# Kernel optimization log

Hardware: AMD Instinct MI355X
Metric: run time of the kernel (lower is better)

## Reference

```python
import jax, jax.numpy as jnp
import numpy as np

DIM = 1024
HEADS = 16
HEAD_DIM = DIM // HEADS


def setup_inputs() -> dict:
    key = jax.random.key(0)
    ks = jax.random.split(key, 5)
    B, N = 4, 2048
    x = jax.random.normal(ks[0], (B, N, DIM), dtype=jnp.float32)
    # nn.Linear default init scale ~ 1/sqrt(fan_in)
    s = 1.0 / np.sqrt(DIM)
    W_qkv = jax.random.uniform(ks[1], (DIM, 3 * DIM), minval=-s, maxval=s, dtype=jnp.float32)
    b_qkv = jax.random.uniform(ks[2], (3 * DIM,), minval=-s, maxval=s, dtype=jnp.float32)
    W_proj = jax.random.uniform(ks[3], (DIM, DIM), minval=-s, maxval=s, dtype=jnp.float32)
    b_proj = jax.random.uniform(ks[4], (DIM,), minval=-s, maxval=s, dtype=jnp.float32)
    return {"x": x, "W_qkv": W_qkv, "b_qkv": b_qkv, "W_proj": W_proj, "b_proj": b_proj}


def reference(x, W_qkv, b_qkv, W_proj, b_proj):
    B, N, C = x.shape
    qkv = x @ W_qkv + b_qkv                      # [B, N, 3C]
    qkv = qkv.reshape(B, N, 3, HEADS, HEAD_DIM)
    q = jnp.transpose(qkv[:, :, 0], (0, 2, 1, 3))  # [B, H, N, D]
    k = jnp.transpose(qkv[:, :, 1], (0, 2, 1, 3))
    v = jnp.transpose(qkv[:, :, 2], (0, 2, 1, 3))
    scale = 1.0 / np.sqrt(HEAD_DIM)
    scores = jnp.einsum('bhqd,bhkd->bhqk', q, k) * scale  # [B, H, N, N]
    attn = jax.nn.softmax(scores, axis=-1)
    out = jnp.einsum('bhqk,bhkd->bhqd', attn, v)           # [B, H, N, D]
    out = jnp.transpose(out, (0, 2, 1, 3)).reshape(B, N, C)
    return out @ W_proj + b_proj
```

## Files before the change

kernel.cpp:

```cpp
#include <hip/hip_runtime.h>

typedef __attribute__((ext_vector_type(2)))  float  f32x2;
typedef __attribute__((ext_vector_type(4)))  float  f32x4;
typedef __attribute__((ext_vector_type(16))) float  f32x16;
typedef __attribute__((ext_vector_type(8)))  short  short8;
typedef __attribute__((ext_vector_type(4)))  unsigned int u32x4;
typedef __attribute__((ext_vector_type(2)))  unsigned int uint2v;

#define MFMA16 __builtin_amdgcn_mfma_f32_16x16x32_bf16
#define MFMA32 __builtin_amdgcn_mfma_f32_32x32x16_bf16

static __device__ __forceinline__ unsigned short f2bf(float f){
  union { float f; unsigned u; } v; v.f = f;
  unsigned r = v.u + 0x7fffu + ((v.u >> 16) & 1u);
  return (unsigned short)(r >> 16);
}

static __device__ __forceinline__ unsigned cvtpk(float a, float b){
  unsigned r;
  asm("v_cvt_pk_bf16_f32 %0, %1, %2" : "=v"(r) : "v"(a), "v"(b));
  return r;
}

static __device__ __forceinline__ void plswap(unsigned &a, unsigned &b){
  asm("v_permlane32_swap_b32 %0, %1" : "+v"(a), "+v"(b));
}

typedef __attribute__((address_space(1))) void gvoid_t;
typedef __attribute__((address_space(3))) void lvoid_t;

static __device__ __forceinline__ void gll16(const unsigned short* g, unsigned short* l){
  __builtin_amdgcn_global_load_lds((gvoid_t*)g, (lvoid_t*)l, 16, 0, 0);
}


__global__ __launch_bounds__(256) void k_convert(const float* __restrict__ x,
                                                 unsigned short* __restrict__ xb){
  __shared__ __align__(16) unsigned short sm[16384];
  const int mblk = blockIdx.x >> 4, kt = blockIdx.x & 15;
  const int t = threadIdx.x;
  const int l16 = t & 15, rg = t >> 4;
  #pragma unroll
  for (int p = 0; p < 16; p++){
    int row = p * 16 + rg;
    f32x4 v = *(const f32x4*)&x[(size_t)(mblk*256 + row) * 1024 + kt*64 + l16*4];
    uint2v u; u[0] = cvtpk(v[0], v[1]); u[1] = cvtpk(v[2], v[3]);
    int g = l16 >> 1;
    *(uint2v*)&sm[row*64 + ((g ^ (row & 7)) << 3) + (l16 & 1)*4] = u;
  }
  __syncthreads();
  size_t obase = (size_t)((mblk*16 + kt)*2) * 8192;
  #pragma unroll
  for (int i = 0; i < 8; i++){
    int o = i * 256 + t;
    int kh = o >> 10, rem = o & 1023;
    int band = rem >> 6, cc = (rem >> 4) & 3, ri = rem & 15;
    int r = band*16 + ri, g = kh*4 + cc;
    short8 vv = *(const short8*)&sm[r*64 + ((g ^ (r & 7)) << 3)];
    *(short8*)&xb[obase + (size_t)kh*8192 + rem*8] = vv;
  }
}

__global__ __launch_bounds__(256) void k_transpose(const float* __restrict__ W,
                                                   unsigned short* __restrict__ Wt,
                                                   int K, int N){
  __shared__ float tile[32][33];
  int n0 = blockIdx.x * 32, k0 = blockIdx.y * 32;
  int tx = threadIdx.x, ty = threadIdx.y;
  #pragma unroll
  for (int r = 0; r < 4; r++)
    tile[ty + 8*r][tx] = W[(size_t)(k0 + ty + 8*r) * N + n0 + tx];
  __syncthreads();
  #pragma unroll
  for (int r = 0; r < 4; r++){
    int nn = ty + 8*r;
    int n = n0 + nn, k = k0 + tx;
    int kt = k >> 6, kh = (k >> 5) & 1, cc = (k >> 3) & 3, ke = k & 7;
    int nblk = n >> 8, band = (n & 255) >> 4, ri = n & 15;
    Wt[(size_t)(((nblk*16 + kt)*2 + kh)) * 8192 + band*512 + cc*128 + ri*8 + ke] =
        f2bf(tile[tx][nn]);
  }
}

#define VMW(N) { __builtin_amdgcn_sched_barrier(0);                        \
                 asm volatile("s_waitcnt vmcnt(" #N ")" ::: "memory");     \
                 __builtin_amdgcn_s_barrier();                             \
                 __builtin_amdgcn_sched_barrier(0); }

template<int MODE>
__global__ __launch_bounds__(512, 2) void k_gemm(const unsigned short* __restrict__ A,
                                                 const unsigned short* __restrict__ Bt,
                                                 const float* __restrict__ bias,
                                                 void* __restrict__ outp,
                                                 int NT){
  __shared__ __align__(16) unsigned short lds[49152];
  const int t = threadIdx.x, w = t >> 6, l = t & 63;
  const int wr = w >> 2, wc = w & 3;
  const int bx = blockIdx.x, by = blockIdx.y;
  const int mblk = bx >> 1, mhalf = bx & 1;

  const unsigned short* Ab = A + (size_t)mblk*262144 + mhalf*4096 + t*8;
  const unsigned short* Bb = Bt + (size_t)by*262144 + t*8;

  f32x4 acc[4][4];
  #pragma unroll
  for (int i = 0; i < 4; i++)
    #pragma unroll
    for (int j = 0; j < 4; j++)
      acc[i][j] = (f32x4){0.f, 0.f, 0.f, 0.f};

  auto stage = [&](int sl){
    const int b = sl & 3;
    const size_t off = (size_t)sl * 8192;
    gll16(Ab + off,        &lds[b*12288 + t*8]);
    gll16(Bb + off,        &lds[b*12288 + 4096 + t*8]);
    gll16(Bb + off + 4096, &lds[b*12288 + 8192 + t*8]);
  };

  auto phase = [&](int b, bool do_stage, int sl){
    short8 af[4], bfr[4];
    const int aoff = b*12288 + wr*2048 + l*8;
    const int boff = b*12288 + 4096 + wc*2048 + l*8;
    #pragma unroll
    for (int i = 0; i < 4; i++) af[i]  = *(const short8*)&lds[aoff + i*512];
    #pragma unroll
    for (int j = 0; j < 4; j++) bfr[j] = *(const short8*)&lds[boff + j*512];
    if (do_stage) stage(sl);
    __builtin_amdgcn_sched_barrier(0);
    __builtin_amdgcn_s_barrier();
    __builtin_amdgcn_s_setprio(1);
    #pragma unroll
    for (int i = 0; i < 4; i++)
      #pragma unroll
      for (int j = 0; j < 4; j++)
        acc[i][j] = MFMA16(af[i], bfr[j], acc[i][j], 0, 0, 0);
    __builtin_amdgcn_s_setprio(0);
  };

  stage(0); stage(1); stage(2);
  VMW(6);

  const int NP = 2 * NT;
  int p = 0;
  for (; p <= NP - 4; ++p){
    phase(p & 3, true, p + 3);
    VMW(6);
  }
  phase(p & 3, false, 0); VMW(3); ++p;
  phase(p & 3, false, 0); VMW(0); ++p;
  phase(p & 3, false, 0);

  if (MODE == 0){
    unsigned short* qg = (unsigned short*)outp;
    unsigned short* kg = qg + (size_t)8388608;
    unsigned short* vg = kg + (size_t)8388608;
    const int which = by >> 2;
    const int lrow = l & 15;
    #pragma unroll
    for (int j = 0; j < 4; j++){
      int col = by*256 + wc*64 + j*16 + lrow;
      float bi = bias[col];
      int cc = col & 1023;
      int h = cc >> 6;
      int d = j*16 + lrow;
      if (which == 2){
        int db = d >> 5, dd = d & 31;
        #pragma unroll
        for (int i = 0; i < 4; i++){
          int nn = bx*128 + wr*64 + i*16 + (l >> 4)*4;
          int b = nn >> 11, key = nn & 2047;
          size_t idx = (size_t)(key >> 6)*4096 + (size_t)(((key >> 4) & 3)*2 + db)*512
                     + (((key >> 3) & 1)*32 + dd)*8 + (key & 7);
          uint2v u;
          u[0] = cvtpk(acc[i][j][0] + bi, acc[i][j][1] + bi);
          u[1] = cvtpk(acc[i][j][2] + bi, acc[i][j][3] + bi);
          *(uint2v*)&vg[(size_t)(b*16 + h)*131072 + idx] = u;
        }
      } else {
        unsigned short* dst = which ? kg : qg;
        float scale = which ? 1.0f : 0.18033688011f;
        int dsub = (d >> 4)*512 + ((d >> 3) & 1)*256 + (d & 7);
        #pragma unroll
        for (int i = 0; i < 4; i++)
          #pragma unroll
          for (int reg = 0; reg < 4; reg++){
            int nn = bx*128 + wr*64 + i*16 + (l >> 4)*4 + reg;
            int b = nn >> 11, row = nn & 2047;
            dst[(size_t)(b*16 + h)*131072 + (size_t)(row >> 5)*2048 + dsub + (row & 31)*8] =
                f2bf((acc[i][j][reg] + bi) * scale);
          }
      }
    }
  } else {
    float* out = (float*)outp;
    #pragma unroll
    for (int i = 0; i < 4; i++)
      #pragma unroll
      for (int reg = 0; reg < 4; reg++){
        int row = bx*128 + wr*64 + i*16 + (l >> 4)*4 + reg;
        #pragma unroll
        for (int j = 0; j < 4; j++){
          int col = by*256 + wc*64 + j*16 + (l & 15);
          out[(size_t)row * 1024 + col] = acc[i][j][reg] + bias[col];
        }
      }
  }
}

__global__ __launch_bounds__(256, 2) void k_attn(const unsigned short* __restrict__ Qg,
                                                 const unsigned short* __restrict__ Kg,
                                                 const unsigned short* __restrict__ Vg,
                                                 unsigned short* __restrict__ aout){
  __shared__ __align__(16) unsigned short lds[20480];

  const int t = threadIdx.x, w = t >> 6, l = t & 63;
  const int hi = l >> 5, q31 = l & 31;
  const int d0 = blockIdx.x;
  const int xcd = d0 & 7, jj = d0 >> 3;
  const int bh = xcd + 8*(jj >> 3);
  const int bx = jj & 7;

  const unsigned short* Qp = Qg + (size_t)bh*131072 + (size_t)bx*16384;
  const unsigned short* Kp = Kg + (size_t)bh*131072;
  const unsigned short* Vp = Vg + (size_t)bh*131072;

  #pragma unroll
  for (int i = 0; i < 8; i++){ int c = i*256 + t; gll16(Qp + c*8, &lds[c*8]); }
  {
    short8 z8 = {0,0,0,0,0,0,0,0};
    *(short8*)&lds[16384 + t*16]     = z8;
    *(short8*)&lds[16384 + t*16 + 8] = z8;
  }
  __syncthreads();
  short8 qf0[4], qf1[4];
  #pragma unroll
  for (int ds = 0; ds < 4; ds++){
    qf0[ds] = *(const short8*)&lds[(2*w + 0)*2048 + ds*512 + l*8];
    qf1[ds] = *(const short8*)&lds[(2*w + 1)*2048 + ds*512 + l*8];
  }
  __syncthreads();

  #pragma unroll
  for (int i = 0; i < 2; i++){
    int c = i*256 + t;
    gll16(Kp + c*8, &lds[c*8]);
    gll16(Vp + c*8, &lds[8192 + c*8]);
  }
  __syncthreads();

  f32x16 ZERO;
  #pragma unroll
  for (int i = 0; i < 16; i++) ZERO[i] = 0.f;
  f32x16 o0lo = ZERO, o0hi = ZERO, o1lo = ZERO, o1hi = ZERO;
  float lsum0 = 0.f, lsum1 = 0.f;
  u32x4 pA0[4], pA1[4], pB0[4], pB1[4];
  #pragma unroll
  for (int ks = 0; ks < 4; ks++){
    pA0[ks][0]=0u; pA0[ks][1]=0u; pA0[ks][2]=0u; pA0[ks][3]=0u;
    pA1[ks][0]=0u; pA1[ks][1]=0u; pA1[ks][2]=0u; pA1[ks][3]=0u;
  }
  int s0 = 0, s1 = 1, s2 = 2;

  auto body = [&](int kt, u32x4 (&pO0)[4], u32x4 (&pO1)[4],
                          u32x4 (&pN0)[4], u32x4 (&pN1)[4]){
    const int cbk = (kt & 1) * 4096;
    if (kt < 31){
      const int nbk = cbk ^ 4096;
      const int nv  = 8192 + s1*4096;
      #pragma unroll
      for (int i = 0; i < 2; i++){
        int c = i*256 + t;
        gll16(Kp + (size_t)(kt + 1)*4096 + c*8, &lds[nbk + c*8]);
        gll16(Vp + (size_t)(kt + 1)*4096 + c*8, &lds[nv + c*8]);
      }
    }

    f32x16 sA0, sB0, sA1, sB1;
    __builtin_amdgcn_s_setprio(1);
    {
      short8 kfA = *(const short8*)&lds[cbk + l*8];
      short8 kfB = *(const short8*)&lds[cbk + 2048 + l*8];
      sA0 = MFMA32(kfA, qf0[0], ZERO, 0, 0, 0);
      sB0 = MFMA32(kfB, qf0[0], ZERO, 0, 0, 0);
      sA1 = MFMA32(kfA, qf1[0], ZERO, 0, 0, 0);
      sB1 = MFMA32(kfB, qf1[0], ZERO, 0, 0, 0);
    }
    #pragma unroll
    for (int ds = 1; ds < 4; ds++){
      short8 kfA = *(const short8*)&lds[cbk + ds*512 + l*8];
      short8 kfB = *(const short8*)&lds[cbk + 2048 + ds*512 + l*8];
      sA0 = MFMA32(kfA, qf0[ds], sA0, 0, 0, 0);
      sB0 = MFMA32(kfB, qf0[ds], sB0, 0, 0, 0);
      sA1 = MFMA32(kfA, qf1[ds], sA1, 0, 0, 0);
      sB1 = MFMA32(kfB, qf1[ds], sB1, 0, 0, 0);
    }
    __builtin_amdgcn_s_setprio(0);
    __builtin_amdgcn_sched_barrier(0);

    const int pvb = 8192 + s2*4096;

    #pragma unroll
    for (int i = 0; i < 16; i++){
      sA0[i] = __builtin_amdgcn_exp2f(sA0[i]);
      sB0[i] = __builtin_amdgcn_exp2f(sB0[i]);
      sA1[i] = __builtin_amdgcn_exp2f(sA1[i]);
      sB1[i] = __builtin_amdgcn_exp2f(sB1[i]);
    }
    lsum0 += ((((sA0[0]+sA0[1])+(sA0[2]+sA0[3])) + ((sA0[4]+sA0[5])+(sA0[6]+sA0[7])))
           +  (((sA0[8]+sA0[9])+(sA0[10]+sA0[11])) + ((sA0[12]+sA0[13])+(sA0[14]+sA0[15]))))
           + ((((sB0[0]+sB0[1])+(sB0[2]+sB0[3])) + ((sB0[4]+sB0[5])+(sB0[6]+sB0[7])))
           +  (((sB0[8]+sB0[9])+(sB0[10]+sB0[11])) + ((sB0[12]+sB0[13])+(sB0[14]+sB0[15]))));
    lsum1 += ((((sA1[0]+sA1[1])+(sA1[2]+sA1[3])) + ((sA1[4]+sA1[5])+(sA1[6]+sA1[7])))
           +  (((sA1[8]+sA1[9])+(sA1[10]+sA1[11])) + ((sA1[12]+sA1[13])+(sA1[14]+sA1[15]))))
           + ((((sB1[0]+sB1[1])+(sB1[2]+sB1[3])) + ((sB1[4]+sB1[5])+(sB1[6]+sB1[7])))
           +  (((sB1[8]+sB1[9])+(sB1[10]+sB1[11])) + ((sB1[12]+sB1[13])+(sB1[14]+sB1[15]))));

    {
      unsigned wA[8], wB[8];
      #pragma unroll
      for (int j = 0; j < 8; j++){ wA[j] = cvtpk(sA0[2*j], sA0[2*j+1]); wB[j] = cvtpk(sB0[2*j], sB0[2*j+1]); }
      { unsigned a=wA[0],b=wA[2]; plswap(a,b); pN0[0][0]=a; pN0[0][2]=b; }
      { unsigned a=wA[1],b=wA[3]; plswap(a,b); pN0[0][1]=a; pN0[0][3]=b; }
      { unsigned a=wA[4],b=wA[6]; plswap(a,b); pN0[1][0]=a; pN0[1][2]=b; }
      { unsigned a=wA[5],b=wA[7]; plswap(a,b); pN0[1][1]=a; pN0[1][3]=b; }
      { unsigned a=wB[0],b=wB[2]; plswap(a,b); pN0[2][0]=a; pN0[2][2]=b; }
      { unsigned a=wB[1],b=wB[3]; plswap(a,b); pN0[2][1]=a; pN0[2][3]=b; }
      { unsigned a=wB[4],b=wB[6]; plswap(a,b); pN0[3][0]=a; pN0[3][2]=b; }
      { unsigned a=wB[5],b=wB[7]; plswap(a,b); pN0[3][1]=a; pN0[3][3]=b; }
    }
    {
      unsigned wA[8], wB[8];
      #pragma unroll
      for (int j = 0; j < 8; j++){ wA[j] = cvtpk(sA1[2*j], sA1[2*j+1]); wB[j] = cvtpk(sB1[2*j], sB1[2*j+1]); }
      { unsigned a=wA[0],b=wA[2]; plswap(a,b); pN1[0][0]=a; pN1[0][2]=b; }
      { unsigned a=wA[1],b=wA[3]; plswap(a,b); pN1[0][1]=a; pN1[0][3]=b; }
      { unsigned a=wA[4],b=wA[6]; plswap(a,b); pN1[1][0]=a; pN1[1][2]=b; }
      { unsigned a=wA[5],b=wA[7]; plswap(a,b); pN1[1][1]=a; pN1[1][3]=b; }
      { unsigned a=wB[0],b=wB[2]; plswap(a,b); pN1[2][0]=a; pN1[2][2]=b; }
      { unsigned a=wB[1],b=wB[3]; plswap(a,b); pN1[2][1]=a; pN1[2][3]=b; }
      { unsigned a=wB[4],b=wB[6]; plswap(a,b); pN1[3][0]=a; pN1[3][2]=b; }
      { unsigned a=wB[5],b=wB[7]; plswap(a,b); pN1[3][1]=a; pN1[3][3]=b; }
    }

    #pragma unroll
    for (int ks = 0; ks < 4; ks++){
      short8 p0r, p1r;
      *(u32x4*)&p0r = pO0[ks];
      *(u32x4*)&p1r = pO1[ks];
      short8 vf0 = *(const short8*)&lds[pvb + (ks*2 + 0)*512 + l*8];
      short8 vf1 = *(const short8*)&lds[pvb + (ks*2 + 1)*512 + l*8];
      o0lo = MFMA32(vf0, p0r, o0lo, 0, 0, 0);
      o0hi = MFMA32(vf1, p0r, o0hi, 0, 0, 0);
      o1lo = MFMA32(vf0, p1r, o1lo, 0, 0, 0);
      o1hi = MFMA32(vf1, p1r, o1hi, 0, 0, 0);
    }

    #pragma unroll
    for (int g4 = 0; g4 < 4; g4++){
      __builtin_amdgcn_sched_group_barrier(0x100, 2, 0);
      __builtin_amdgcn_sched_group_barrier(0x002, 40, 0);
      __builtin_amdgcn_sched_group_barrier(0x008, 4, 0);
    }
    __builtin_amdgcn_sched_group_barrier(0x002, 64, 0);

    __syncthreads();
    int tmp = s2; s2 = s0; s0 = s1; s1 = tmp;
  };

  for (int kt2 = 0; kt2 < 32; kt2 += 2){
    body(kt2,     pA0, pA1, pB0, pB1);
    body(kt2 + 1, pB0, pB1, pA0, pA1);
  }

  {
    const int pvb = 8192 + s2*4096;
    __builtin_amdgcn_s_setprio(1);
    #pragma unroll
    for (int ks = 0; ks < 4; ks++){
      short8 p0r, p1r;
      *(u32x4*)&p0r = pA0[ks];
      *(u32x4*)&p1r = pA1[ks];
      short8 vf0 = *(const short8*)&lds[pvb + (ks*2 + 0)*512 + l*8];
      short8 vf1 = *(const short8*)&lds[pvb + (ks*2 + 1)*512 + l*8];
      o0lo = MFMA32(vf0, p0r, o0lo, 0, 0, 0);
      o0hi = MFMA32(vf1, p0r, o0hi, 0, 0, 0);
      o1lo = MFMA32(vf0, p1r, o1lo, 0, 0, 0);
      o1hi = MFMA32(vf1, p1r, o1hi, 0, 0, 0);
    }
    __builtin_amdgcn_s_setprio(0);
  }
  __syncthreads();

  lsum0 += __shfl_xor(lsum0, 32);
  lsum1 += __shfl_xor(lsum1, 32);
  {
    float inv0 = 1.0f / lsum0, inv1 = 1.0f / lsum1;
    int qr0 = w*64 + q31, qr1 = w*64 + 32 + q31;
    #pragma unroll
    for (int j = 0; j < 8; j++){
      int dd0 = 8*(j >> 1) + 2*(j & 1) + 4*hi;
      int dd1 = dd0 + 32;
      *(unsigned*)&lds[qr0*64 + (((dd0 >> 3) ^ (qr0 & 7)) << 3) + (dd0 & 7)] =
          cvtpk(o0lo[2*j] * inv0, o0lo[2*j+1] * inv0);
      *(unsigned*)&lds[qr0*64 + (((dd1 >> 3) ^ (qr0 & 7)) << 3) + (dd1 & 7)] =
          cvtpk(o0hi[2*j] * inv0, o0hi[2*j+1] * inv0);
      *(unsigned*)&lds[qr1*64 + (((dd0 >> 3) ^ (qr1 & 7)) << 3) + (dd0 & 7)] =
          cvtpk(o1lo[2*j] * inv1, o1lo[2*j+1] * inv1);
      *(unsigned*)&lds[qr1*64 + (((dd1 >> 3) ^ (qr1 & 7)) << 3) + (dd1 & 7)] =
          cvtpk(o1hi[2*j] * inv1, o1hi[2*j+1] * inv1);
    }
  }
  __syncthreads();
  {
    int mblk = (bh >> 4)*8 + bx;
    int h = bh & 15;
    #pragma unroll
    for (int i = 0; i < 8; i++){
      int idx = i*256 + t;
      int kh = idx >> 10, rem = idx & 1023;
      int band = rem >> 6, cc = (rem >> 4) & 3, ri = rem & 15;
      int r = band*16 + ri, g = kh*4 + cc;
      short8 vv = *(const short8*)&lds[r*64 + ((g ^ (r & 7)) << 3)];
      size_t chunk = (size_t)((mblk*16 + h)*2 + kh);
      *(short8*)&aout[chunk*8192 + (size_t)band*512 + cc*128 + ri*8] = vv;
    }
  }
}

extern "C" void kernel_launch(void* const* d_in, const int* in_sizes, int n_in,
                              void* d_out, int out_size, void* d_ws, size_t ws_size,
                              hipStream_t stream){
  const float* x     = (const float*)d_in[0];
  const float* Wqkv  = (const float*)d_in[1];
  const float* bqkv  = (const float*)d_in[2];
  const float* Wproj = (const float*)d_in[3];
  const float* bproj = (const float*)d_in[4];

  unsigned short* ws   = (unsigned short*)d_ws;
  unsigned short* xb   = ws;
  unsigned short* Wqt  = ws + (size_t)8192 * 1024;
  unsigned short* Wpt  = Wqt + (size_t)3072 * 1024;
  unsigned short* qkvb = Wpt + (size_t)1024 * 1024;

  k_convert<<<512, 256, 0, stream>>>(x, xb);
  k_transpose<<<dim3(96, 32), dim3(32, 8), 0, stream>>>(Wqkv, Wqt, 1024, 3072);
  k_transpose<<<dim3(32, 32), dim3(32, 8), 0, stream>>>(Wproj, Wpt, 1024, 1024);
  k_gemm<0><<<dim3(64, 12), 512, 0, stream>>>(xb, Wqt, bqkv, qkvb, 16);
  k_attn<<<512, 256, 0, stream>>>(qkvb, qkvb + (size_t)8388608,
                                  qkvb + (size_t)16777216, xb);
  k_gemm<1><<<dim3(64, 4), 512, 0, stream>>>(xb, Wpt, bproj, (void*)d_out, 16);
}
```

Measured before the change: 165.4 us.

## Merge prep kernels into one launch and shrink GEMM pipeline to three stages

Folds the x conversion and both weight transposes into one k_prep kernel, removing two launches and the gaps between them. The GEMM's LDS ring buffer drops from four stages to three (72KB instead of 96KB), and launch bounds are raised to allow four blocks per CU, trading prefetch depth for occupancy. The shallower prefetch may expose more memory latency, and the higher occupancy target may squeeze registers for the 64-float accumulator. The k_prep blocks also now reserve 32KB of LDS where the transpose blocks previously used much less.

```diff
diff --git a/kernel.cpp b/kernel.cpp
--- a/kernel.cpp
+++ b/kernel.cpp
@@ -34,51 +34,57 @@
 }
 
 
-__global__ __launch_bounds__(256) void k_convert(const float* __restrict__ x,
-                                                 unsigned short* __restrict__ xb){
-  __shared__ __align__(16) unsigned short sm[16384];
-  const int mblk = blockIdx.x >> 4, kt = blockIdx.x & 15;
-  const int t = threadIdx.x;
-  const int l16 = t & 15, rg = t >> 4;
-  #pragma unroll
-  for (int p = 0; p < 16; p++){
-    int row = p * 16 + rg;
-    f32x4 v = *(const f32x4*)&x[(size_t)(mblk*256 + row) * 1024 + kt*64 + l16*4];
-    uint2v u; u[0] = cvtpk(v[0], v[1]); u[1] = cvtpk(v[2], v[3]);
-    int g = l16 >> 1;
-    *(uint2v*)&sm[row*64 + ((g ^ (row & 7)) << 3) + (l16 & 1)*4] = u;
-  }
-  __syncthreads();
-  size_t obase = (size_t)((mblk*16 + kt)*2) * 8192;
-  #pragma unroll
-  for (int i = 0; i < 8; i++){
-    int o = i * 256 + t;
-    int kh = o >> 10, rem = o & 1023;
-    int band = rem >> 6, cc = (rem >> 4) & 3, ri = rem & 15;
-    int r = band*16 + ri, g = kh*4 + cc;
-    short8 vv = *(const short8*)&sm[r*64 + ((g ^ (r & 7)) << 3)];
-    *(short8*)&xb[obase + (size_t)kh*8192 + rem*8] = vv;
-  }
-}
-
-__global__ __launch_bounds__(256) void k_transpose(const float* __restrict__ W,
-                                                   unsigned short* __restrict__ Wt,
-                                                   int K, int N){
-  __shared__ float tile[32][33];
-  int n0 = blockIdx.x * 32, k0 = blockIdx.y * 32;
-  int tx = threadIdx.x, ty = threadIdx.y;
-  #pragma unroll
-  for (int r = 0; r < 4; r++)
-    tile[ty + 8*r][tx] = W[(size_t)(k0 + ty + 8*r) * N + n0 + tx];
-  __syncthreads();
-  #pragma unroll
-  for (int r = 0; r < 4; r++){
-    int nn = ty + 8*r;
-    int n = n0 + nn, k = k0 + tx;
-    int kt = k >> 6, kh = (k >> 5) & 1, cc = (k >> 3) & 3, ke = k & 7;
-    int nblk = n >> 8, band = (n & 255) >> 4, ri = n & 15;
-    Wt[(size_t)(((nblk*16 + kt)*2 + kh)) * 8192 + band*512 + cc*128 + ri*8 + ke] =
-        f2bf(tile[tx][nn]);
+__global__ __launch_bounds__(256) void k_prep(const float* __restrict__ x,
+                                              unsigned short* __restrict__ xb,
+                                              const float* __restrict__ Wq,
+                                              unsigned short* __restrict__ Wqt,
+                                              const float* __restrict__ Wp,
+                                              unsigned short* __restrict__ Wpt){
+  __shared__ __align__(16) unsigned char smraw[32768];
+  const int bid = blockIdx.x, t = threadIdx.x;
+  if (bid < 512){
+    unsigned short* sm = (unsigned short*)smraw;
+    const int mblk = bid >> 4, kt = bid & 15;
+    const int l16 = t & 15, rg = t >> 4;
+    #pragma unroll
+    for (int p = 0; p < 16; p++){
+      int row = p * 16 + rg;
+      f32x4 v = *(const f32x4*)&x[(size_t)(mblk*256 + row) * 1024 + kt*64 + l16*4];
+      uint2v u; u[0] = cvtpk(v[0], v[1]); u[1] = cvtpk(v[2], v[3]);
+      int g = l16 >> 1;
+      *(uint2v*)&sm[row*64 + ((g ^ (row & 7)) << 3) + (l16 & 1)*4] = u;
+    }
+    __syncthreads();
+    size_t obase = (size_t)((mblk*16 + kt)*2) * 8192;
+    #pragma unroll
+    for (int i = 0; i < 8; i++){
+      int o = i * 256 + t;
+      int kh = o >> 10, rem = o & 1023;
+      int band = rem >> 6, cc = (rem >> 4) & 3, ri = rem & 15;
+      int r = band*16 + ri, g = kh*4 + cc;
+      short8 vv = *(const short8*)&sm[r*64 + ((g ^ (r & 7)) << 3)];
+      *(short8*)&xb[obase + (size_t)kh*8192 + rem*8] = vv;
+    }
+  } else {
+    float (*tile)[33] = (float(*)[33])smraw;
+    int wid = bid - 512;
+    const float* W; unsigned short* Wt; int N, n0, k0;
+    if (wid < 3072){ W = Wq; Wt = Wqt; N = 3072; n0 = (wid % 96)*32; k0 = (wid / 96)*32; }
+    else { wid -= 3072; W = Wp; Wt = Wpt; N = 1024; n0 = (wid & 31)*32; k0 = (wid >> 5)*32; }
+    const int tx = t & 31, ty = t >> 5;
+    #pragma unroll
+    for (int r = 0; r < 4; r++)
+      tile[ty + 8*r][tx] = W[(size_t)(k0 + ty + 8*r) * N + n0 + tx];
+    __syncthreads();
+    #pragma unroll
+    for (int r = 0; r < 4; r++){
+      int nn = ty + 8*r;
+      int n = n0 + nn, k = k0 + tx;
+      int kt = k >> 6, kh = (k >> 5) & 1, cc = (k >> 3) & 3, ke = k & 7;
+      int nblk = n >> 8, band = (n & 255) >> 4, ri = n & 15;
+      Wt[(size_t)(((nblk*16 + kt)*2 + kh)) * 8192 + band*512 + cc*128 + ri*8 + ke] =
+          f2bf(tile[tx][nn]);
+    }
   }
 }
 
@@ -88,12 +94,12 @@
                  __builtin_amdgcn_sched_barrier(0); }
 
 template<int MODE>
-__global__ __launch_bounds__(512, 2) void k_gemm(const unsigned short* __restrict__ A,
+__global__ __launch_bounds__(512, 4) void k_gemm(const unsigned short* __restrict__ A,
                                                  const unsigned short* __restrict__ Bt,
                                                  const float* __restrict__ bias,
                                                  void* __restrict__ outp,
                                                  int NT){
-  __shared__ __align__(16) unsigned short lds[49152];
+  __shared__ __align__(16) unsigned short lds[36864];
   const int t = threadIdx.x, w = t >> 6, l = t & 63;
   const int wr = w >> 2, wc = w & 3;
   const int bx = blockIdx.x, by = blockIdx.y;
@@ -110,7 +116,7 @@
       acc[i][j] = (f32x4){0.f, 0.f, 0.f, 0.f};
 
   auto stage = [&](int sl){
-    const int b = sl & 3;
+    const int b = sl % 3;
     const size_t off = (size_t)sl * 8192;
     gll16(Ab + off,        &lds[b*12288 + t*8]);
     gll16(Bb + off,        &lds[b*12288 + 4096 + t*8]);
@@ -137,18 +143,17 @@
     __builtin_amdgcn_s_setprio(0);
   };
 
-  stage(0); stage(1); stage(2);
-  VMW(6);
+  stage(0); stage(1);
+  VMW(3);
 
   const int NP = 2 * NT;
   int p = 0;
-  for (; p <= NP - 4; ++p){
-    phase(p & 3, true, p + 3);
-    VMW(6);
-  }
-  phase(p & 3, false, 0); VMW(3); ++p;
-  phase(p & 3, false, 0); VMW(0); ++p;
-  phase(p & 3, false, 0);
+  for (; p <= NP - 3; ++p){
+    phase(p % 3, true, p + 2);
+    VMW(3);
+  }
+  phase(p % 3, false, 0); VMW(0); ++p;
+  phase(p % 3, false, 0);
 
   if (MODE == 0){
     unsigned short* qg = (unsigned short*)outp;
@@ -442,9 +447,7 @@
   unsigned short* Wpt  = Wqt + (size_t)3072 * 1024;
   unsigned short* qkvb = Wpt + (size_t)1024 * 1024;
 
-  k_convert<<<512, 256, 0, stream>>>(x, xb);
-  k_transpose<<<dim3(96, 32), dim3(32, 8), 0, stream>>>(Wqkv, Wqt, 1024, 3072);
-  k_transpose<<<dim3(32, 32), dim3(32, 8), 0, stream>>>(Wproj, Wpt, 1024, 1024);
+  k_prep<<<4608, 256, 0, stream>>>(x, xb, Wqkv, Wqt, Wproj, Wpt);
   k_gemm<0><<<dim3(64, 12), 512, 0, stream>>>(xb, Wqt, bqkv, qkvb, 16);
   k_attn<<<512, 256, 0, stream>>>(qkvb, qkvb + (size_t)8388608,
                                   qkvb + (size_t)16777216, xb);
```

Result: faster. 155.0 us (-6.3%).
